# Kernel tuning notes

Hardware: AMD Instinct MI355X
Metric: run time of the kernel (lower is better)

The kernel has to match this reference:

```python
import jax, jax.numpy as jnp
import numpy as np

NUM_HEADS = 16
D_K = 64
BATCH_SIZE = 64
NUM_EDGES = 32768


def setup_inputs() -> dict:
    key = jax.random.key(0)
    k1, k2, k3, k4 = jax.random.split(key, 4)
    global_query = jax.random.normal(k1, (NUM_HEADS, BATCH_SIZE, D_K), dtype=jnp.float32)
    local_key = jax.random.normal(k2, (NUM_HEADS, NUM_EDGES, D_K), dtype=jnp.float32)
    local_value = jax.random.normal(k3, (NUM_HEADS, NUM_EDGES, D_K), dtype=jnp.float32)
    batch = jnp.sort(jax.random.randint(k4, (NUM_EDGES,), 0, BATCH_SIZE, dtype=jnp.int64))
    return {"global_query": global_query, "local_key": local_key,
            "local_value": local_value, "batch": batch}


def reference(global_query, local_key, local_value, batch):
    # global_query: [h, b, d]; local_key/value: [h, e, d]; batch: [e] segment ids
    num_heads, batch_size, d_k = global_query.shape
    # seg[b, e] = True iff edge e belongs to graph b
    seg = batch[None, :] == jnp.arange(batch_size, dtype=batch.dtype)[:, None]  # [b, e]
    # NOTE: original module does NOT scale by sqrt(d_k) despite its name
    scores = jnp.einsum('hbd,hed->hbe', global_query, local_key)  # [h, b, e]
    # per-segment softmax: out-of-segment entries get -inf -> exactly 0 weight,
    # matching the original which only softmaxes over edges with batch == i
    masked = jnp.where(seg[None, :, :], scores, -jnp.inf)
    attn = jax.nn.softmax(masked, axis=-1)  # [h, b, e]; zeros outside segment
    output = jnp.einsum('hbe,hed->hbd', attn, local_value)  # [h, b, d]
    return output, attn
```

## Files before the change

kernel.cpp:

```cpp
#include <hip/hip_runtime.h>
#include <math.h>

#define NH 16
#define NB 64
#define DK 64
#define NE 32768
#define BLOCK 512

typedef float vf4 __attribute__((ext_vector_type(4)));

__global__ void seg_bounds_kernel(const int* __restrict__ batch, int* __restrict__ bounds) {
    int e = blockIdx.x * 256 + threadIdx.x;
    if (e >= NE) return;
    int be = batch[e];
    if (e == 0) {
        for (int b = 0; b <= be; ++b) bounds[b] = 0;
    } else {
        int bp = batch[e - 1];
        for (int b = bp + 1; b <= be; ++b) bounds[b] = e;
    }
    if (e == NE - 1) {
        for (int b = be + 1; b <= NB; ++b) bounds[b] = NE;
    }
}

__global__ __launch_bounds__(BLOCK) void sdpa_seg_kernel(
    const float* __restrict__ Q,
    const float* __restrict__ K,
    const float* __restrict__ V,
    const int*   __restrict__ bounds,
    float* __restrict__ out,
    float* __restrict__ attn,
    float* __restrict__ ksc_base)
{
    const int b    = blockIdx.x;
    const int h    = blockIdx.y;
    const int tid  = threadIdx.x;
    const int wave = tid >> 6;
    const int lane = tid & 63;

    const int start = bounds[b];
    const int end   = bounds[b + 1];

    float* arow = attn + ((size_t)h * NB + b) * NE;
    float* ksc  = ksc_base + (size_t)h * NE;

    __shared__ float qs[DK];
    __shared__ float sm[8], sl[8];
    __shared__ float red[8][DK];

    if (tid < DK) qs[tid] = Q[((size_t)h * NB + b) * DK + tid];

    {
        vf4 z4 = (vf4)(0.f);
        vf4* arow4 = (vf4*)arow;
        for (int i = tid; i < NE / 4; i += BLOCK)
            __builtin_nontemporal_store(z4, arow4 + i);
    }
    __syncthreads();

    const float4* q4 = (const float4*)qs;
    float m = -INFINITY, l = 0.f;
    for (int e = start + tid; e < end; e += BLOCK) {
        const float4* kr = (const float4*)(K + ((size_t)h * NE + e) * DK);
        float sx = 0.f, sy = 0.f, sz = 0.f, sw = 0.f;
        #pragma unroll
        for (int i = 0; i < DK / 4; ++i) {
            float4 kv = kr[i];
            float4 qv = q4[i];
            sx = fmaf(kv.x, qv.x, sx);
            sy = fmaf(kv.y, qv.y, sy);
            sz = fmaf(kv.z, qv.z, sz);
            sw = fmaf(kv.w, qv.w, sw);
        }
        float s = (sx + sy) + (sz + sw);
        ksc[e] = s;
        float nm = fmaxf(m, s);
        l = l * __expf(m - nm) + __expf(s - nm);
        m = nm;
    }

    #pragma unroll
    for (int off = 32; off; off >>= 1) {
        float om = __shfl_xor(m, off);
        float ol = __shfl_xor(l, off);
        float nm = fmaxf(m, om);
        float t1 = (l  > 0.f) ? l  * __expf(m  - nm) : 0.f;
        float t2 = (ol > 0.f) ? ol * __expf(om - nm) : 0.f;
        m = nm; l = t1 + t2;
    }
    if (lane == 0) { sm[wave] = m; sl[wave] = l; }
    __syncthreads();

    float M = -INFINITY;
    #pragma unroll
    for (int w = 0; w < 8; ++w) M = fmaxf(M, sm[w]);
    float L = 0.f;
    #pragma unroll
    for (int w = 0; w < 8; ++w) L += (sl[w] > 0.f) ? sl[w] * __expf(sm[w] - M) : 0.f;
    const float inv = (L > 0.f) ? 1.f / L : 0.f;

    for (int e = start + tid; e < end; e += BLOCK)
        __builtin_nontemporal_store(__expf(ksc[e] - M) * inv, arow + e);

    const int S   = end - start;
    const int per = (S + 7) >> 3;
    const int cb  = start + wave * per;
    const int ce  = (cb + per < end) ? cb + per : end;

    float a0 = 0.f, a1 = 0.f, a2 = 0.f, a3 = 0.f;
    int e = cb;
    for (; e + 3 < ce; e += 4) {
        float p0 = __expf(ksc[e]     - M) * inv;
        float p1 = __expf(ksc[e + 1] - M) * inv;
        float p2 = __expf(ksc[e + 2] - M) * inv;
        float p3 = __expf(ksc[e + 3] - M) * inv;
        const float* vb = V + ((size_t)h * NE + e) * DK + lane;
        a0 = fmaf(p0, vb[0 * DK], a0);
        a1 = fmaf(p1, vb[1 * DK], a1);
        a2 = fmaf(p2, vb[2 * DK], a2);
        a3 = fmaf(p3, vb[3 * DK], a3);
    }
    for (; e < ce; ++e) {
        float p = __expf(ksc[e] - M) * inv;
        a0 = fmaf(p, V[((size_t)h * NE + e) * DK + lane], a0);
    }
    red[wave][lane] = (a0 + a1) + (a2 + a3);
    __syncthreads();
    if (wave == 0) {
        float r = 0.f;
        #pragma unroll
        for (int w = 0; w < 8; ++w) r += red[w][lane];
        out[((size_t)h * NB + b) * DK + lane] = r;
    }
}

extern "C" void kernel_launch(void* const* d_in, const int* in_sizes, int n_in,
                              void* d_out, int out_size, void* d_ws, size_t ws_size,
                              hipStream_t stream) {
    const float* Q     = (const float*)d_in[0];
    const float* K     = (const float*)d_in[1];
    const float* V     = (const float*)d_in[2];
    const int*   batch = (const int*)d_in[3];

    float* out  = (float*)d_out;
    float* attn = out + (size_t)NH * NB * DK;

    int*   bounds = (int*)d_ws;
    float* ksc    = (float*)d_ws + 128;

    seg_bounds_kernel<<<NE / 256, 256, 0, stream>>>(batch, bounds);

    dim3 grid(NB, NH);
    sdpa_seg_kernel<<<grid, BLOCK, 0, stream>>>(Q, K, V, bounds, out, attn, ksc);
}
```

Baseline: 339.5 us.

## Split zero-fill into separate blocks and use 16-lane cooperative QK/PV rows

Launches twice as many blocks. Odd blocks only zero-fill the parts of each attention row that lie outside the segment, and even blocks compute that row's segment softmax and output. The compute path now has 16 lanes cooperate on each key or value row with coalesced float4 loads and shuffle reductions, replacing the old scheme of one thread per key with strided row reads. The block shrinks to 256 threads with an occupancy hint. The aim is better memory coalescing and overlap of the zero-fill bandwidth with compute. The cost is extra shuffle work and more blocks.

```diff
diff --git a/kernel.cpp b/kernel.cpp
--- a/kernel.cpp
+++ b/kernel.cpp
@@ -5,7 +5,8 @@
 #define NB 64
 #define DK 64
 #define NE 32768
-#define BLOCK 512
+#define NHB (NH * NB)
+#define TPB 256
 
 typedef float vf4 __attribute__((ext_vector_type(4)));
 
@@ -24,7 +25,7 @@
     }
 }
 
-__global__ __launch_bounds__(BLOCK) void sdpa_seg_kernel(
+__global__ __launch_bounds__(TPB, 8) void sdpa_fused(
     const float* __restrict__ Q,
     const float* __restrict__ K,
     const float* __restrict__ V,
@@ -33,55 +34,75 @@
     float* __restrict__ attn,
     float* __restrict__ ksc_base)
 {
-    const int b    = blockIdx.x;
-    const int h    = blockIdx.y;
-    const int tid  = threadIdx.x;
+    const int bid = blockIdx.x;
+    const int tid = threadIdx.x;
+
+    if (bid & 1) {
+        const int row   = bid >> 1;
+        const int b     = row & (NB - 1);
+        const int start = bounds[b];
+        const int end   = bounds[b + 1];
+        float* arow = attn + (size_t)row * NE;
+        vf4 z4 = {0.f, 0.f, 0.f, 0.f};
+        vf4* a4 = (vf4*)arow;
+        const int c1 = start >> 2;
+        for (int i = tid; i < c1; i += TPB)
+            __builtin_nontemporal_store(z4, a4 + i);
+        for (int i = ((end + 3) >> 2) + tid; i < NE / 4; i += TPB)
+            __builtin_nontemporal_store(z4, a4 + i);
+        if (tid < (start & 3))
+            __builtin_nontemporal_store(0.f, arow + (start & ~3) + tid);
+        if (tid < ((4 - (end & 3)) & 3))
+            __builtin_nontemporal_store(0.f, arow + end + tid);
+        return;
+    }
+
+    const int row  = bid >> 1;
+    const int h    = row >> 6;
+    const int b    = row & (NB - 1);
     const int wave = tid >> 6;
     const int lane = tid & 63;
+    const int esub = lane >> 4;
+    const int dsub = (lane & 15) << 2;
 
     const int start = bounds[b];
     const int end   = bounds[b + 1];
 
+    const float* Kh  = K + (size_t)h * NE * DK;
+    const float* Vh  = V + (size_t)h * NE * DK;
+    float* ksc  = ksc_base + (size_t)h * NE;
     float* arow = attn + ((size_t)h * NB + b) * NE;
-    float* ksc  = ksc_base + (size_t)h * NE;
 
-    __shared__ float qs[DK];
-    __shared__ float sm[8], sl[8];
-    __shared__ float red[8][DK];
+    const vf4 q4 = *(const vf4*)(Q + ((size_t)h * NB + b) * DK + dsub);
 
-    if (tid < DK) qs[tid] = Q[((size_t)h * NB + b) * DK + tid];
+    const int S   = end - start;
+    const int per = (S + 3) >> 2;
+    const int cb  = start + wave * per;
+    const int ce  = (cb + per < end) ? cb + per : end;
 
-    {
-        vf4 z4 = (vf4)(0.f);
-        vf4* arow4 = (vf4*)arow;
-        for (int i = tid; i < NE / 4; i += BLOCK)
-            __builtin_nontemporal_store(z4, arow4 + i);
+    __shared__ float sm[4], sl[4];
+    __shared__ vf4 red[4][16];
+
+    float m = -INFINITY, l = 0.f;
+    for (int e0 = cb; e0 < ce; e0 += 4) {
+        const int  eg  = e0 + esub;
+        const bool act = (eg < ce);
+        const int  ec  = act ? eg : (ce - 1);
+        vf4 kv = *(const vf4*)(Kh + (size_t)ec * DK + dsub);
+        float s = fmaf(kv.x, q4.x, fmaf(kv.y, q4.y, fmaf(kv.z, q4.z, kv.w * q4.w)));
+        s += __shfl_xor(s, 1);
+        s += __shfl_xor(s, 2);
+        s += __shfl_xor(s, 4);
+        s += __shfl_xor(s, 8);
+        if (act) {
+            if ((lane & 15) == 0) ksc[eg] = s;
+            float nm = fmaxf(m, s);
+            l = l * __expf(m - nm) + __expf(s - nm);
+            m = nm;
+        }
     }
-    __syncthreads();
-
-    const float4* q4 = (const float4*)qs;
-    float m = -INFINITY, l = 0.f;
-    for (int e = start + tid; e < end; e += BLOCK) {
-        const float4* kr = (const float4*)(K + ((size_t)h * NE + e) * DK);
-        float sx = 0.f, sy = 0.f, sz = 0.f, sw = 0.f;
-        #pragma unroll
-        for (int i = 0; i < DK / 4; ++i) {
-            float4 kv = kr[i];
-            float4 qv = q4[i];
-            sx = fmaf(kv.x, qv.x, sx);
-            sy = fmaf(kv.y, qv.y, sy);
-            sz = fmaf(kv.z, qv.z, sz);
-            sw = fmaf(kv.w, qv.w, sw);
-        }
-        float s = (sx + sy) + (sz + sw);
-        ksc[e] = s;
-        float nm = fmaxf(m, s);
-        l = l * __expf(m - nm) + __expf(s - nm);
-        m = nm;
-    }
-
     #pragma unroll
-    for (int off = 32; off; off >>= 1) {
+    for (int off = 16; off <= 32; off <<= 1) {
         float om = __shfl_xor(m, off);
         float ol = __shfl_xor(l, off);
         float nm = fmaxf(m, om);
@@ -92,46 +113,46 @@
     if (lane == 0) { sm[wave] = m; sl[wave] = l; }
     __syncthreads();
 
-    float M = -INFINITY;
-    #pragma unroll
-    for (int w = 0; w < 8; ++w) M = fmaxf(M, sm[w]);
+    float M = fmaxf(fmaxf(sm[0], sm[1]), fmaxf(sm[2], sm[3]));
     float L = 0.f;
     #pragma unroll
-    for (int w = 0; w < 8; ++w) L += (sl[w] > 0.f) ? sl[w] * __expf(sm[w] - M) : 0.f;
+    for (int w = 0; w < 4; ++w)
+        L += (sl[w] > 0.f) ? sl[w] * __expf(sm[w] - M) : 0.f;
     const float inv = (L > 0.f) ? 1.f / L : 0.f;
 
-    for (int e = start + tid; e < end; e += BLOCK)
+    for (int e = start + tid; e < end; e += TPB)
         __builtin_nontemporal_store(__expf(ksc[e] - M) * inv, arow + e);
 
-    const int S   = end - start;
-    const int per = (S + 7) >> 3;
-    const int cb  = start + wave * per;
-    const int ce  = (cb + per < end) ? cb + per : end;
-
-    float a0 = 0.f, a1 = 0.f, a2 = 0.f, a3 = 0.f;
-    int e = cb;
-    for (; e + 3 < ce; e += 4) {
-        float p0 = __expf(ksc[e]     - M) * inv;
-        float p1 = __expf(ksc[e + 1] - M) * inv;
-        float p2 = __expf(ksc[e + 2] - M) * inv;
-        float p3 = __expf(ksc[e + 3] - M) * inv;
-        const float* vb = V + ((size_t)h * NE + e) * DK + lane;
-        a0 = fmaf(p0, vb[0 * DK], a0);
-        a1 = fmaf(p1, vb[1 * DK], a1);
-        a2 = fmaf(p2, vb[2 * DK], a2);
-        a3 = fmaf(p3, vb[3 * DK], a3);
+    vf4 acc = {0.f, 0.f, 0.f, 0.f};
+    for (int e0 = cb; e0 < ce; e0 += 4) {
+        const int  eg  = e0 + esub;
+        const bool act = (eg < ce);
+        const int  ec  = act ? eg : (ce - 1);
+        float sv = ksc[ec];
+        float p  = act ? (__expf(sv - M) * inv) : 0.f;
+        vf4 vv = *(const vf4*)(Vh + (size_t)ec * DK + dsub);
+        acc.x = fmaf(p, vv.x, acc.x);
+        acc.y = fmaf(p, vv.y, acc.y);
+        acc.z = fmaf(p, vv.z, acc.z);
+        acc.w = fmaf(p, vv.w, acc.w);
     }
-    for (; e < ce; ++e) {
-        float p = __expf(ksc[e] - M) * inv;
-        a0 = fmaf(p, V[((size_t)h * NE + e) * DK + lane], a0);
+    #pragma unroll
+    for (int off = 16; off <= 32; off <<= 1) {
+        acc.x += __shfl_xor(acc.x, off);
+        acc.y += __shfl_xor(acc.y, off);
+        acc.z += __shfl_xor(acc.z, off);
+        acc.w += __shfl_xor(acc.w, off);
     }
-    red[wave][lane] = (a0 + a1) + (a2 + a3);
+    if (lane < 16) red[wave][lane] = acc;
     __syncthreads();
-    if (wave == 0) {
-        float r = 0.f;
-        #pragma unroll
-        for (int w = 0; w < 8; ++w) r += red[w][lane];
-        out[((size_t)h * NB + b) * DK + lane] = r;
+    if (wave == 0 && lane < 16) {
+        vf4 r = red[0][lane];
+        vf4 r1 = red[1][lane], r2 = red[2][lane], r3 = red[3][lane];
+        r.x += r1.x + r2.x + r3.x;
+        r.y += r1.y + r2.y + r3.y;
+        r.z += r1.z + r2.z + r3.z;
+        r.w += r1.w + r2.w + r3.w;
+        *(vf4*)(out + ((size_t)h * NB + b) * DK + (lane << 2)) = r;
     }
 }
 
@@ -151,6 +172,5 @@
 
     seg_bounds_kernel<<<NE / 256, 256, 0, stream>>>(batch, bounds);
 
-    dim3 grid(NB, NH);
-    sdpa_seg_kernel<<<grid, BLOCK, 0, stream>>>(Q, K, V, bounds, out, attn, ksc);
+    sdpa_fused<<<2 * NHB, TPB, 0, stream>>>(Q, K, V, bounds, out, attn, ksc);
 }
```

Result: slower. 359.9 us (+6.0%).

## Split attention into separate zero, score and finalize kernels

Applied to the files above, without the earlier changes.

Replaces the single per-(graph, head) kernel with three passes. A grid-stride kernel zeroes the whole attention matrix, a fully parallel kernel computes every edge's QK score using its own batch id, and a finalize kernel does a two-pass max/sum softmax followed by the V reduction, unrolled 8 ways with nontemporal loads. This spreads the K dot products across all CUs instead of one block per uneven segment, at the cost of extra launches and an extra read of the score buffer.

```diff
diff --git a/kernel.cpp b/kernel.cpp
--- a/kernel.cpp
+++ b/kernel.cpp
@@ -5,7 +5,8 @@
 #define NB 64
 #define DK 64
 #define NE 32768
-#define BLOCK 512
+#define TPB 256
+#define TPF 512
 
 typedef float vf4 __attribute__((ext_vector_type(4)));
 
@@ -24,14 +25,46 @@
     }
 }
 
-__global__ __launch_bounds__(BLOCK) void sdpa_seg_kernel(
+__global__ __launch_bounds__(TPB) void attn_zero_kernel(float* __restrict__ attn) {
+    vf4 z = {0.f, 0.f, 0.f, 0.f};
+    vf4* a4 = (vf4*)attn;
+    const size_t n4 = (size_t)NH * NB * NE / 4;
+    size_t i = (size_t)blockIdx.x * TPB + threadIdx.x;
+    const size_t stride = (size_t)gridDim.x * TPB;
+    for (; i < n4; i += stride)
+        __builtin_nontemporal_store(z, a4 + i);
+}
+
+__global__ __launch_bounds__(TPB) void scores_kernel(
     const float* __restrict__ Q,
     const float* __restrict__ K,
+    const int*   __restrict__ batch,
+    float* __restrict__ ksc)
+{
+    const int h = blockIdx.x >> 7;
+    const int e = ((blockIdx.x & 127) << 8) + threadIdx.x;
+    const int b = batch[e];
+    const vf4* qrow = (const vf4*)(Q + ((size_t)h * NB + b) * DK);
+    const vf4* krow = (const vf4*)(K + ((size_t)h * NE + e) * DK);
+    float s0 = 0.f, s1 = 0.f, s2 = 0.f, s3 = 0.f;
+    #pragma unroll
+    for (int j = 0; j < DK / 4; ++j) {
+        vf4 kv = __builtin_nontemporal_load(krow + j);
+        vf4 qv = qrow[j];
+        s0 = fmaf(kv.x, qv.x, s0);
+        s1 = fmaf(kv.y, qv.y, s1);
+        s2 = fmaf(kv.z, qv.z, s2);
+        s3 = fmaf(kv.w, qv.w, s3);
+    }
+    ksc[(size_t)h * NE + e] = (s0 + s1) + (s2 + s3);
+}
+
+__global__ __launch_bounds__(TPF) void finalize_kernel(
     const float* __restrict__ V,
     const int*   __restrict__ bounds,
+    const float* __restrict__ ksc_base,
     float* __restrict__ out,
-    float* __restrict__ attn,
-    float* __restrict__ ksc_base)
+    float* __restrict__ attn)
 {
     const int b    = blockIdx.x;
     const int h    = blockIdx.y;
@@ -42,90 +75,67 @@
     const int start = bounds[b];
     const int end   = bounds[b + 1];
 
-    float* arow = attn + ((size_t)h * NB + b) * NE;
-    float* ksc  = ksc_base + (size_t)h * NE;
+    const float* ksc  = ksc_base + (size_t)h * NE;
+    float*       arow = attn + ((size_t)h * NB + b) * NE;
 
-    __shared__ float qs[DK];
-    __shared__ float sm[8], sl[8];
+    __shared__ float smax[8], ssum[8];
     __shared__ float red[8][DK];
 
-    if (tid < DK) qs[tid] = Q[((size_t)h * NB + b) * DK + tid];
-
-    {
-        vf4 z4 = (vf4)(0.f);
-        vf4* arow4 = (vf4*)arow;
-        for (int i = tid; i < NE / 4; i += BLOCK)
-            __builtin_nontemporal_store(z4, arow4 + i);
-    }
+    float m = -INFINITY;
+    for (int e = start + tid; e < end; e += TPF) m = fmaxf(m, ksc[e]);
+    #pragma unroll
+    for (int off = 32; off; off >>= 1) m = fmaxf(m, __shfl_xor(m, off));
+    if (lane == 0) smax[wave] = m;
     __syncthreads();
-
-    const float4* q4 = (const float4*)qs;
-    float m = -INFINITY, l = 0.f;
-    for (int e = start + tid; e < end; e += BLOCK) {
-        const float4* kr = (const float4*)(K + ((size_t)h * NE + e) * DK);
-        float sx = 0.f, sy = 0.f, sz = 0.f, sw = 0.f;
-        #pragma unroll
-        for (int i = 0; i < DK / 4; ++i) {
-            float4 kv = kr[i];
-            float4 qv = q4[i];
-            sx = fmaf(kv.x, qv.x, sx);
-            sy = fmaf(kv.y, qv.y, sy);
-            sz = fmaf(kv.z, qv.z, sz);
-            sw = fmaf(kv.w, qv.w, sw);
-        }
-        float s = (sx + sy) + (sz + sw);
-        ksc[e] = s;
-        float nm = fmaxf(m, s);
-        l = l * __expf(m - nm) + __expf(s - nm);
-        m = nm;
-    }
-
-    #pragma unroll
-    for (int off = 32; off; off >>= 1) {
-        float om = __shfl_xor(m, off);
-        float ol = __shfl_xor(l, off);
-        float nm = fmaxf(m, om);
-        float t1 = (l  > 0.f) ? l  * __expf(m  - nm) : 0.f;
-        float t2 = (ol > 0.f) ? ol * __expf(om - nm) : 0.f;
-        m = nm; l = t1 + t2;
-    }
-    if (lane == 0) { sm[wave] = m; sl[wave] = l; }
-    __syncthreads();
-
     float M = -INFINITY;
     #pragma unroll
-    for (int w = 0; w < 8; ++w) M = fmaxf(M, sm[w]);
+    for (int w = 0; w < 8; ++w) M = fmaxf(M, smax[w]);
+
+    float l = 0.f;
+    for (int e = start + tid; e < end; e += TPF) l += __expf(ksc[e] - M);
+    #pragma unroll
+    for (int off = 32; off; off >>= 1) l += __shfl_xor(l, off);
+    if (lane == 0) ssum[wave] = l;
+    __syncthreads();
     float L = 0.f;
     #pragma unroll
-    for (int w = 0; w < 8; ++w) L += (sl[w] > 0.f) ? sl[w] * __expf(sm[w] - M) : 0.f;
+    for (int w = 0; w < 8; ++w) L += ssum[w];
     const float inv = (L > 0.f) ? 1.f / L : 0.f;
 
-    for (int e = start + tid; e < end; e += BLOCK)
+    for (int e = start + tid; e < end; e += TPF)
         __builtin_nontemporal_store(__expf(ksc[e] - M) * inv, arow + e);
 
     const int S   = end - start;
     const int per = (S + 7) >> 3;
     const int cb  = start + wave * per;
-    const int ce  = (cb + per < end) ? cb + per : end;
+    int ce = cb + per; if (ce > end) ce = end;
 
-    float a0 = 0.f, a1 = 0.f, a2 = 0.f, a3 = 0.f;
+    float a0=0.f,a1=0.f,a2=0.f,a3=0.f,a4=0.f,a5=0.f,a6=0.f,a7=0.f;
     int e = cb;
-    for (; e + 3 < ce; e += 4) {
-        float p0 = __expf(ksc[e]     - M) * inv;
-        float p1 = __expf(ksc[e + 1] - M) * inv;
-        float p2 = __expf(ksc[e + 2] - M) * inv;
-        float p3 = __expf(ksc[e + 3] - M) * inv;
+    for (; e + 7 < ce; e += 8) {
+        float p0 = __expf(ksc[e+0] - M) * inv;
+        float p1 = __expf(ksc[e+1] - M) * inv;
+        float p2 = __expf(ksc[e+2] - M) * inv;
+        float p3 = __expf(ksc[e+3] - M) * inv;
+        float p4 = __expf(ksc[e+4] - M) * inv;
+        float p5 = __expf(ksc[e+5] - M) * inv;
+        float p6 = __expf(ksc[e+6] - M) * inv;
+        float p7 = __expf(ksc[e+7] - M) * inv;
         const float* vb = V + ((size_t)h * NE + e) * DK + lane;
-        a0 = fmaf(p0, vb[0 * DK], a0);
-        a1 = fmaf(p1, vb[1 * DK], a1);
-        a2 = fmaf(p2, vb[2 * DK], a2);
-        a3 = fmaf(p3, vb[3 * DK], a3);
+        a0 = fmaf(p0, __builtin_nontemporal_load(vb + 0*DK), a0);
+        a1 = fmaf(p1, __builtin_nontemporal_load(vb + 1*DK), a1);
+        a2 = fmaf(p2, __builtin_nontemporal_load(vb + 2*DK), a2);
+        a3 = fmaf(p3, __builtin_nontemporal_load(vb + 3*DK), a3);
+        a4 = fmaf(p4, __builtin_nontemporal_load(vb + 4*DK), a4);
+        a5 = fmaf(p5, __builtin_nontemporal_load(vb + 5*DK), a5);
+        a6 = fmaf(p6, __builtin_nontemporal_load(vb + 6*DK), a6);
+        a7 = fmaf(p7, __builtin_nontemporal_load(vb + 7*DK), a7);
     }
     for (; e < ce; ++e) {
         float p = __expf(ksc[e] - M) * inv;
-        a0 = fmaf(p, V[((size_t)h * NE + e) * DK + lane], a0);
+        a0 = fmaf(p, __builtin_nontemporal_load(V + ((size_t)h * NE + e) * DK + lane), a0);
     }
-    red[wave][lane] = (a0 + a1) + (a2 + a3);
+    red[wave][lane] = ((a0 + a1) + (a2 + a3)) + ((a4 + a5) + (a6 + a7));
     __syncthreads();
     if (wave == 0) {
         float r = 0.f;
@@ -150,7 +160,8 @@
     float* ksc    = (float*)d_ws + 128;
 
     seg_bounds_kernel<<<NE / 256, 256, 0, stream>>>(batch, bounds);
-
-    dim3 grid(NB, NH);
-    sdpa_seg_kernel<<<grid, BLOCK, 0, stream>>>(Q, K, V, bounds, out, attn, ksc);
+    attn_zero_kernel<<<2048, TPB, 0, stream>>>(attn);
+    scores_kernel<<<NH * (NE / TPB), TPB, 0, stream>>>(Q, K, batch, ksc);
+    dim3 fgrid(NB, NH);
+    finalize_kernel<<<fgrid, TPF, 0, stream>>>(V, bounds, ksc, out, attn);
 }
```

Measured after the change: 372.6 us. 1.1x slower.
